# Kernel tuning notes

Hardware: AMD Instinct MI355X
Metric: run time of the kernel (lower is better)

Reference implementation:

```python
import jax, jax.numpy as jnp
import numpy as np

# Model constants (from init_kwargs)
B, S, D = 2, 2048, 2048          # batch, seq, d_model
E = 64                           # num_routed_experts
TOP_K = 4
BOT = int(D * 0.25)              # bottle_dim = 512
EXP = 1536                       # routed expert hidden (bigmac_expert_size)
DFF = 8192                       # shared expert hidden (d_ff)
Z_LOSS_W = 1e-4
MOE_SCALE = 0.5                  # 1/(1 + [num_shared_experts>0])


def setup_inputs() -> dict:
    key = jax.random.key(0)
    ks = jax.random.split(key, 10)
    std = 0.011
    return {
        "x": jax.random.normal(ks[0], (B, S, D), jnp.float32),
        "router_w": jax.random.normal(ks[1], (E, D), jnp.float32) * 0.02,
        "gate_w": jax.random.normal(ks[2], (DFF, D), jnp.float32) * std,
        "up_w": jax.random.normal(ks[3], (DFF, D), jnp.float32) * std,
        "down_w": jax.random.normal(ks[4], (D, DFF), jnp.float32) * std,
        "w_down": jax.random.normal(ks[5], (BOT, D), jnp.float32) * std,
        "w_up": jax.random.normal(ks[6], (D, BOT), jnp.float32) * std,
        "w12": jax.random.normal(ks[7], (E, BOT, 2 * EXP), jnp.float32) * std,
        "w3": jax.random.normal(ks[8], (E, EXP, BOT), jnp.float32) * std,
    }


def reference(x, router_w, gate_w, up_w, down_w, w_down, w_up, w12, w3):
    b, s, d = x.shape
    h = x.reshape(-1, d)                       # [N, D]
    N = h.shape[0]
    NT = N * TOP_K                             # total routed token-slots

    # ---- router (fp32) ----
    logits = h @ router_w.T                    # [N, E]
    scores = jax.nn.sigmoid(logits)
    z_loss = jnp.mean(jnp.nan_to_num(logits) ** 2) * Z_LOSS_W
    # expert_bias is None -> selection_scores == scores
    _, topk_idx = jax.lax.top_k(scores, TOP_K)             # [N, K]
    topk_logits = jnp.take_along_axis(logits, topk_idx, axis=1)
    gating = jax.nn.softmax(topk_logits, axis=-1)          # [N, K]

    # ---- shared expert (SwiGLU) ----
    shared = (jax.nn.silu(h @ gate_w.T) * (h @ up_w.T)) @ down_w.T  # [N, D]

    # ---- bottleneck down-projection ----
    down = h @ w_down.T                        # [N, BOT]

    # ---- dispatch: sort tokens by expert, capacity-limited padding ----
    flat = topk_idx.reshape(-1)                # [NT]
    order = jnp.argsort(flat)                  # stable sort
    sorted_e = flat[order]
    counts = jax.ops.segment_sum(jnp.ones(NT, jnp.int32), flat, num_segments=E)
    ptr = jnp.cumsum(counts) - counts          # expert start offsets
    local = jnp.arange(NT) - ptr[sorted_e]     # rank within expert
    max_load = (NT // E // 8 + 6) * 8          # capacity per expert
    num_slots = E * max_load
    mask = local < max_load
    slots = sorted_e * max_load + local
    token_idx = jnp.repeat(jnp.arange(N), TOP_K)

    # reverse_map[slot] = source token row (N = dummy row); extra slot absorbs dropped tokens
    rev = jnp.full(num_slots + 1, N, dtype=jnp.int32)
    rev = rev.at[jnp.where(mask, slots, num_slots)].set(token_idx[order].astype(jnp.int32))
    rev = rev[:num_slots]

    h_dummy = jnp.concatenate([down, jnp.zeros((1, BOT), down.dtype)], axis=0)
    padding = h_dummy[rev].reshape(E, max_load, BOT)

    # ---- grouped expert GEMMs ----
    h12 = jnp.einsum('eld,edf->elf', padding, w12)   # [E, max_load, 2*EXP]
    h1, h2 = jnp.split(h12, 2, axis=-1)
    po = jnp.einsum('elf,efd->eld', jax.nn.silu(h1) * h2, w3)  # [E, max_load, BOT]
    po = jnp.concatenate([po.reshape(-1, BOT), jnp.zeros((1, BOT), po.dtype)], axis=0)

    # ---- combine: gather back, weight by gating ----
    gm = jnp.full(NT, num_slots, dtype=jnp.int32)
    gm = gm.at[order].set(jnp.where(mask, slots, num_slots).astype(jnp.int32))
    gathered = po[gm].reshape(N, TOP_K, BOT)
    routed = jnp.einsum('nk,nkd->nd', gating, gathered) @ w_up.T  # [N, D]

    # eval mode: route_scale = 1.0, aux_loss = 0
    out = ((shared + routed) * MOE_SCALE).reshape(b, s, d)
    return out, z_loss
```

## Files before the change

### kernel.cpp

```cpp
#include <hip/hip_runtime.h>

#define DEV __device__ __forceinline__

typedef __attribute__((ext_vector_type(4))) float f4;
typedef __attribute__((ext_vector_type(8))) __bf16 bfrag;
typedef __attribute__((ext_vector_type(4))) unsigned short us4;
typedef __attribute__((ext_vector_type(8))) unsigned short us8;

#define NTOK   4096
#define DMODEL 2048
#define NEXP   64
#define MAXLD  304
#define NSLOT  19456

DEV unsigned short f2bf(float f){
  union { float f; unsigned int i; } u; u.f = f;
  unsigned int r = u.i + 0x7fffu + ((u.i >> 16) & 1u);
  return (unsigned short)(r >> 16);
}
DEV float bf2f(unsigned short b){
  union { unsigned int i; float f; } u; u.i = ((unsigned int)b) << 16;
  return u.f;
}

DEV void gl_lds16(const unsigned short* g, unsigned short* l){
  __builtin_amdgcn_global_load_lds(
      (const __attribute__((address_space(1))) void*)g,
      (__attribute__((address_space(3))) void*)l, 16, 0, 0);
}

template<int EPI>
__global__ __launch_bounds__(256) void gemm_bt(
    const unsigned short* __restrict__ A, const unsigned short* __restrict__ B,
    void* __restrict__ Cp, const float* __restrict__ addin,
    int M, int N, int K, long long sA, long long sB, long long sC)
{
  __shared__ unsigned short As[128*32];
  __shared__ unsigned short Bs[128*32];
  A += (long long)blockIdx.z * sA;
  B += (long long)blockIdx.z * sB;
  const long long cbase = (long long)blockIdx.z * sC;
  const int bm = blockIdx.y * 128, bn = blockIdx.x * 128;
  const int t = threadIdx.x, wave = t >> 6, lane = t & 63;
  const int wm = (wave >> 1) * 64, wn = (wave & 1) * 64;
  const int fr = lane & 15, kg = lane >> 4;

  f4 acc[4][4];
#pragma unroll
  for (int m = 0; m < 4; ++m)
#pragma unroll
    for (int n = 0; n < 4; ++n)
      acc[m][n] = f4{0.f, 0.f, 0.f, 0.f};

  const int i0 = t, i1 = 256 + t;
  int ar0 = bm + (i0 >> 2); if (ar0 > M - 1) ar0 = M - 1;
  int ar1 = bm + (i1 >> 2); if (ar1 > M - 1) ar1 = M - 1;
  int br0 = bn + (i0 >> 2); if (br0 > N - 1) br0 = N - 1;
  int br1 = bn + (i1 >> 2); if (br1 > N - 1) br1 = N - 1;
  const unsigned short* ap0 = A + (long long)ar0 * K + (i0 & 3) * 8;
  const unsigned short* ap1 = A + (long long)ar1 * K + (i1 & 3) * 8;
  const unsigned short* bp0 = B + (long long)br0 * K + (i0 & 3) * 8;
  const unsigned short* bp1 = B + (long long)br1 * K + (i1 & 3) * 8;
  unsigned short* da0 = As + wave * 512;
  unsigned short* da1 = As + 2048 + wave * 512;
  unsigned short* db0 = Bs + wave * 512;
  unsigned short* db1 = Bs + 2048 + wave * 512;

  for (int k0 = 0; k0 < K; k0 += 32){
    gl_lds16(ap0, da0);
    gl_lds16(ap1, da1);
    gl_lds16(bp0, db0);
    gl_lds16(bp1, db1);
    ap0 += 32; ap1 += 32; bp0 += 32; bp1 += 32;
    __syncthreads();
    bfrag af[4], bfv[4];
#pragma unroll
    for (int m = 0; m < 4; ++m) af[m] = *(const bfrag*)&As[(wm + m*16 + fr)*32 + kg*8];
#pragma unroll
    for (int n = 0; n < 4; ++n) bfv[n] = *(const bfrag*)&Bs[(wn + n*16 + fr)*32 + kg*8];
#pragma unroll
    for (int m = 0; m < 4; ++m)
#pragma unroll
      for (int n = 0; n < 4; ++n)
        acc[m][n] = __builtin_amdgcn_mfma_f32_16x16x32_bf16(af[m], bfv[n], acc[m][n], 0, 0, 0);
    __syncthreads();
  }

#pragma unroll
  for (int m = 0; m < 4; ++m){
    const int row0 = bm + wm + m*16 + kg*4;
#pragma unroll
    for (int n = 0; n < 4; ++n){
      const int col = bn + wn + n*16 + fr;
      if (col < N){
        f4 v = acc[m][n];
#pragma unroll
        for (int r = 0; r < 4; ++r){
          const int row = row0 + r;
          if (row < M){
            const long long off = cbase + (long long)row * N + col;
            if (EPI == 0)      ((unsigned short*)Cp)[off] = f2bf(v[r]);
            else if (EPI == 1) ((float*)Cp)[off] = v[r];
            else               ((float*)Cp)[off] = (v[r] + addin[off]) * 0.5f;
          }
        }
      }
    }
  }
}

__global__ void cvt_bf16(const float* __restrict__ in, unsigned short* __restrict__ out,
                         long long n4)
{
  long long i = (long long)blockIdx.x * 256 + threadIdx.x;
  if (i >= n4) return;
  float4 v = ((const float4*)in)[i];
  us4 o; o[0] = f2bf(v.x); o[1] = f2bf(v.y); o[2] = f2bf(v.z); o[3] = f2bf(v.w);
  ((us4*)out)[i] = o;
}

__global__ __launch_bounds__(256) void transpose_cvt(const float* __restrict__ in,
    unsigned short* __restrict__ out, int R, int C)
{
  __shared__ float tile[32][33];
  const long long z = blockIdx.z;
  const float* ip = in + z * (long long)R * C;
  unsigned short* op = out + z * (long long)R * C;
  const int r0 = blockIdx.y * 32, c0 = blockIdx.x * 32;
  const int t = threadIdx.x;
  const int lr = t >> 3, lc = (t & 7) * 4;
  float4 v = *(const float4*)(ip + (long long)(r0 + lr) * C + c0 + lc);
  tile[lr][lc+0] = v.x; tile[lr][lc+1] = v.y; tile[lr][lc+2] = v.z; tile[lr][lc+3] = v.w;
  __syncthreads();
  const int oc = t >> 3, orr = (t & 7) * 4;
  us4 o;
  o[0] = f2bf(tile[orr+0][oc]); o[1] = f2bf(tile[orr+1][oc]);
  o[2] = f2bf(tile[orr+2][oc]); o[3] = f2bf(tile[orr+3][oc]);
  *(us4*)(op + (long long)(c0 + oc) * R + r0 + orr) = o;
}

__global__ void router_topk(const float* __restrict__ logits, int* __restrict__ topk,
                            float* __restrict__ gating, float* __restrict__ zout)
{
  const int t = threadIdx.x, w = t >> 6, lane = t & 63;
  const int n = blockIdx.x * 4 + w;
  const float lg = logits[(long long)n * 64 + lane];
  float z = lg * lg;
#pragma unroll
  for (int off = 32; off; off >>= 1) z += __shfl_xor(z, off);
  __shared__ float zs[4];
  if (lane == 0) zs[w] = z;
  __syncthreads();
  if (t == 0) atomicAdd(zout, (zs[0]+zs[1]+zs[2]+zs[3]) * (0.0001f / 262144.0f));

  float cur = lg;
  float tl[4]; int ti[4];
#pragma unroll
  for (int k = 0; k < 4; ++k){
    float s = cur; int si = lane;
#pragma unroll
    for (int off = 32; off; off >>= 1){
      float so = __shfl_xor(s, off); int io = __shfl_xor(si, off);
      if (so > s || (so == s && io < si)){ s = so; si = io; }
    }
    tl[k] = s; ti[k] = si;
    if (lane == si) cur = -3.0e38f;
  }
  if (lane == 0){
    const float m0 = tl[0];
    const float e0 = __expf(tl[0]-m0), e1 = __expf(tl[1]-m0),
                e2 = __expf(tl[2]-m0), e3 = __expf(tl[3]-m0);
    const float inv = 1.0f / (e0 + e1 + e2 + e3);
    topk[n*4+0] = ti[0]; topk[n*4+1] = ti[1]; topk[n*4+2] = ti[2]; topk[n*4+3] = ti[3];
    gating[n*4+0] = e0*inv; gating[n*4+1] = e1*inv; gating[n*4+2] = e2*inv; gating[n*4+3] = e3*inv;
  }
}

__global__ void scan_route(const int* __restrict__ topk, int* __restrict__ gm,
                           int* __restrict__ rev, int* __restrict__ counts)
{
  const int e = blockIdx.x;
  const int t = threadIdx.x, w = t >> 6, lane = t & 63;
  __shared__ int wtot[4];
  int running = 0;
  for (int c = 0; c < 16384; c += 256){
    const int j = c + t;
    const bool p = (topk[j] == e);
    const unsigned long long m = __ballot(p);
    const int prefix = __popcll(m & ((1ull << lane) - 1ull));
    if (lane == 0) wtot[w] = __popcll(m);
    __syncthreads();
    int woff = 0;
#pragma unroll
    for (int i = 0; i < 4; ++i){ if (i < w) woff += wtot[i]; }
    const int btot = wtot[0] + wtot[1] + wtot[2] + wtot[3];
    if (p){
      const int rank = running + woff + prefix;
      gm[j] = (rank < MAXLD) ? (e * MAXLD + rank) : NSLOT;
      if (rank < MAXLD) rev[e * MAXLD + rank] = j >> 2;
    }
    running += btot;
    __syncthreads();
  }
  if (t == 0) counts[e] = running;
}

__global__ void gather_pad(const unsigned short* __restrict__ down, const int* __restrict__ rev,
                           const int* __restrict__ counts, unsigned short* __restrict__ pad)
{
  const int idx = blockIdx.x * 256 + threadIdx.x;
  const int s = idx >> 6, c8 = (idx & 63) * 8;
  const int e = s / MAXLD;
  const int r = s - e * MAXLD;
  int cnt = counts[e]; if (cnt > MAXLD) cnt = MAXLD;
  us8 v = {0,0,0,0,0,0,0,0};
  if (r < cnt){
    const int tok = rev[s];
    v = *(const us8*)(down + (long long)tok * 512 + c8);
  }
  *(us8*)(pad + (long long)s * 512 + c8) = v;
}

__global__ void silu_mul(const unsigned short* __restrict__ G, const unsigned short* __restrict__ U,
                         unsigned short* __restrict__ O, long long ldg, long long ldu, long long ldo,
                         long long cols8, long long total)
{
  const long long idx = (long long)blockIdx.x * 256 + threadIdx.x;
  if (idx >= total) return;
  const long long rr = idx / cols8;
  const long long cc = (idx - rr * cols8) * 8;
  us8 g = *(const us8*)(G + rr * ldg + cc);
  us8 u = *(const us8*)(U + rr * ldu + cc);
  us8 o;
#pragma unroll
  for (int j = 0; j < 8; ++j){
    const float gf = bf2f(g[j]);
    const float s = gf / (1.0f + __expf(-gf));
    o[j] = f2bf(s * bf2f(u[j]));
  }
  *(us8*)(O + rr * ldo + cc) = o;
}

__global__ void combine_moe(const unsigned short* __restrict__ po, const int* __restrict__ gm,
                            const float* __restrict__ gating, unsigned short* __restrict__ routed)
{
  const int idx = blockIdx.x * 256 + threadIdx.x;
  const int n = idx >> 6, c8 = (idx & 63) * 8;
  float acc[8] = {0,0,0,0,0,0,0,0};
#pragma unroll
  for (int k = 0; k < 4; ++k){
    const int slot = gm[n*4 + k];
    if (slot < NSLOT){
      const float gw = gating[n*4 + k];
      us8 v = *(const us8*)(po + (long long)slot * 512 + c8);
#pragma unroll
      for (int j = 0; j < 8; ++j) acc[j] += gw * bf2f(v[j]);
    }
  }
  us8 o;
#pragma unroll
  for (int j = 0; j < 8; ++j) o[j] = f2bf(acc[j]);
  *(us8*)(routed + (long long)n * 512 + c8) = o;
}

extern "C" void kernel_launch(void* const* d_in, const int* in_sizes, int n_in,
                              void* d_out, int out_size, void* d_ws, size_t ws_size,
                              hipStream_t stream)
{
  const float* x      = (const float*)d_in[0];
  const float* rw     = (const float*)d_in[1];
  const float* gate_w = (const float*)d_in[2];
  const float* up_w   = (const float*)d_in[3];
  const float* down_w = (const float*)d_in[4];
  const float* w_down = (const float*)d_in[5];
  const float* w_up   = (const float*)d_in[6];
  const float* w12    = (const float*)d_in[7];
  const float* w3     = (const float*)d_in[8];
  float* out = (float*)d_out;

  char* ws = (char*)d_ws;
  unsigned short* HBF   = (unsigned short*)(ws + 0ull);
  unsigned short* RWBF  = (unsigned short*)(ws + 16777216ull);
  unsigned short* GATEB = (unsigned short*)(ws + 17039360ull);
  unsigned short* UPB   = (unsigned short*)(ws + 50593792ull);
  unsigned short* DWB   = (unsigned short*)(ws + 84148224ull);
  unsigned short* WDB   = (unsigned short*)(ws + 117702656ull);
  unsigned short* WUB   = (unsigned short*)(ws + 119799808ull);
  unsigned short* W12T  = (unsigned short*)(ws + 121896960ull);
  unsigned short* W3T   = (unsigned short*)(ws + 323223552ull);
  float*          LOGIT = (float*)(ws + 423886848ull);
  int*            TOPKI = (int*)(ws + 424935424ull);
  float*          GATE4 = (float*)(ws + 425000960ull);
  int*            GM    = (int*)(ws + 425066496ull);
  int*            CNT   = (int*)(ws + 425132032ull);
  int*            REV   = (int*)(ws + 425132288ull);
  unsigned short* GU    = (unsigned short*)(ws + 425210112ull);
  unsigned short* ACTS  = (unsigned short*)(ws + 559427840ull);
  float*          SHRD  = (float*)(ws + 626536704ull);
  unsigned short* DNB   = (unsigned short*)(ws + 660091136ull);
  unsigned short* PAD   = (unsigned short*)(ws + 664285440ull);
  unsigned short* PO    = (unsigned short*)(ws + 684208384ull);
  unsigned short* RTD   = (unsigned short*)(ws + 704131328ull);

  hipMemsetAsync((char*)d_out + 8388608ull * 4, 0, 4, stream);

  cvt_bf16<<<8192,  256, 0, stream>>>(x,      HBF,   2097152);
  cvt_bf16<<<128,   256, 0, stream>>>(rw,     RWBF,  32768);
  cvt_bf16<<<16384, 256, 0, stream>>>(gate_w, GATEB, 4194304);
  cvt_bf16<<<16384, 256, 0, stream>>>(up_w,   UPB,   4194304);
  cvt_bf16<<<16384, 256, 0, stream>>>(down_w, DWB,   4194304);
  cvt_bf16<<<1024,  256, 0, stream>>>(w_down, WDB,   262144);
  cvt_bf16<<<1024,  256, 0, stream>>>(w_up,   WUB,   262144);
  transpose_cvt<<<dim3(96,16,64), 256, 0, stream>>>(w12, W12T, 512, 3072);
  transpose_cvt<<<dim3(16,48,64), 256, 0, stream>>>(w3,  W3T,  1536, 512);

  gemm_bt<1><<<dim3(1,32,1), 256, 0, stream>>>(HBF, RWBF, LOGIT, nullptr,
                                               4096, 64, 2048, 0, 0, 0);
  router_topk<<<1024, 256, 0, stream>>>(LOGIT, TOPKI, GATE4, out + 8388608);
  scan_route<<<64, 256, 0, stream>>>(TOPKI, GM, REV, CNT);

  gemm_bt<0><<<dim3(64,32,1), 256, 0, stream>>>(HBF, GATEB, GU, nullptr,
                                                4096, 8192, 2048, 0, 0, 0);
  gemm_bt<0><<<dim3(64,32,1), 256, 0, stream>>>(HBF, UPB, GU + 33554432ull, nullptr,
                                                4096, 8192, 2048, 0, 0, 0);
  silu_mul<<<16384, 256, 0, stream>>>(GU, GU + 33554432ull, ACTS, 8192, 8192, 8192,
                                      1024, 4194304);
  gemm_bt<1><<<dim3(16,32,1), 256, 0, stream>>>(ACTS, DWB, SHRD, nullptr,
                                                4096, 2048, 8192, 0, 0, 0);

  gemm_bt<0><<<dim3(4,32,1), 256, 0, stream>>>(HBF, WDB, DNB, nullptr,
                                               4096, 512, 2048, 0, 0, 0);
  gather_pad<<<4864, 256, 0, stream>>>(DNB, REV, CNT, PAD);
  gemm_bt<0><<<dim3(24,3,64), 256, 0, stream>>>(PAD, W12T, GU, nullptr,
                                                304, 3072, 512, 155648, 1572864, 933888);
  silu_mul<<<14592, 256, 0, stream>>>(GU, GU + 1536, ACTS, 3072, 3072, 1536,
                                      192, 3735552);
  gemm_bt<0><<<dim3(4,3,64), 256, 0, stream>>>(ACTS, W3T, PO, nullptr,
                                               304, 512, 1536, 466944, 786432, 155648);
  combine_moe<<<1024, 256, 0, stream>>>(PO, GM, GATE4, RTD);

  gemm_bt<2><<<dim3(16,32,1), 256, 0, stream>>>(RTD, WUB, out, SHRD,
                                                4096, 2048, 512, 0, 0, 0);
}
```

Baseline: 1.346 ms.

## Add 256x256-tile triple-buffered GEMM kernel for shared-expert projections

Introduces a new 512-thread GEMM with 256x256 output tiles, a three-stage LDS ring fed by global_load_lds, XOR-swizzled LDS layout, grid remapping for L2 locality, and MFMA priority hints. It replaces the 128x128 GEMM for the three large shared-expert SwiGLU matmuls. The larger tiles raise arithmetic intensity and the deeper pipeline overlaps loads with MFMA. In exchange it uses heavy register and LDS pressure (96KB LDS per block), and the down-projection grid shrinks to 128 blocks, which may underfill the CUs.

Result: faster. 1.261 ms (-6.3%).

```diff
diff --git a/kernel.cpp b/kernel.cpp
--- a/kernel.cpp
+++ b/kernel.cpp
@@ -27,6 +27,130 @@
   __builtin_amdgcn_global_load_lds(
       (const __attribute__((address_space(1))) void*)g,
       (__attribute__((address_space(3))) void*)l, 16, 0, 0);
+}
+
+template<int EPI>
+__global__ __launch_bounds__(512, 2) void gemm256(
+    const unsigned short* __restrict__ A, const unsigned short* __restrict__ B,
+    void* __restrict__ Cp, int M, int N, int K)
+{
+  __shared__ unsigned short As[3][256*32];
+  __shared__ unsigned short Bs[3][256*32];
+
+  const int nwg = gridDim.x * gridDim.y;
+  int bid = blockIdx.y * gridDim.x + blockIdx.x;
+  bid = (bid & 7) * (nwg >> 3) + (bid >> 3);
+  const int bx = bid % gridDim.x, by = bid / gridDim.x;
+  const int bm = by * 256, bn = bx * 256;
+
+  const int t = threadIdx.x, lane = t & 63;
+  const int wave = t >> 6;
+  const int wm = (wave >> 2) * 128, wn = (wave & 3) * 64;
+  const int fr = lane & 15, kg = lane >> 4;
+
+  const int p0 = t, p1 = t + 512;
+  const int ar0 = p0 >> 2, as0 = (p0 & 3) ^ ((ar0 >> 1) & 3);
+  const int ar1 = p1 >> 2, as1 = (p1 & 3) ^ ((ar1 >> 1) & 3);
+  const unsigned short* a0 = A + (long long)(bm + ar0) * K + as0 * 8;
+  const unsigned short* a1 = A + (long long)(bm + ar1) * K + as1 * 8;
+  const unsigned short* b0 = B + (long long)(bn + ar0) * K + as0 * 8;
+  const unsigned short* b1 = B + (long long)(bn + ar1) * K + as1 * 8;
+
+  f4 acc[8][4];
+#pragma unroll
+  for (int m = 0; m < 8; ++m)
+#pragma unroll
+    for (int n = 0; n < 4; ++n) acc[m][n] = f4{0.f,0.f,0.f,0.f};
+
+  const int nt = K >> 5;
+
+  gl_lds16(a0, &As[0][p0*8]); gl_lds16(a1, &As[0][p1*8]);
+  gl_lds16(b0, &Bs[0][p0*8]); gl_lds16(b1, &Bs[0][p1*8]);
+  a0 += 32; a1 += 32; b0 += 32; b1 += 32;
+  gl_lds16(a0, &As[1][p0*8]); gl_lds16(a1, &As[1][p1*8]);
+  gl_lds16(b0, &Bs[1][p0*8]); gl_lds16(b1, &Bs[1][p1*8]);
+  a0 += 32; a1 += 32; b0 += 32; b1 += 32;
+  asm volatile("s_waitcnt vmcnt(4)" ::: "memory");
+  __builtin_amdgcn_s_barrier();
+  __builtin_amdgcn_sched_barrier(0);
+
+  int cur = 0;
+  for (int tt = 0; tt < nt; ++tt){
+    const unsigned short* Ab = As[cur];
+    const unsigned short* Bb = Bs[cur];
+    const int stg = (cur >= 1) ? cur - 1 : cur + 2;
+    const bool do_stage = (tt + 2 < nt);
+
+    bfrag bf[4];
+#pragma unroll
+    for (int n = 0; n < 4; ++n){
+      const int r = wn + n*16 + fr;
+      bf[n] = *(const bfrag*)&Bb[r*32 + ((kg ^ ((r>>1)&3)) << 3)];
+    }
+
+    bfrag af[4];
+#pragma unroll
+    for (int m = 0; m < 4; ++m){
+      const int r = wm + m*16 + fr;
+      af[m] = *(const bfrag*)&Ab[r*32 + ((kg ^ ((r>>1)&3)) << 3)];
+    }
+    if (do_stage){
+      gl_lds16(a0, &As[stg][p0*8]); gl_lds16(a1, &As[stg][p1*8]);
+      a0 += 32; a1 += 32;
+    }
+    __builtin_amdgcn_s_setprio(1);
+#pragma unroll
+    for (int m = 0; m < 4; ++m)
+#pragma unroll
+      for (int n = 0; n < 4; ++n)
+        acc[m][n] = __builtin_amdgcn_mfma_f32_16x16x32_bf16(af[m], bf[n], acc[m][n], 0, 0, 0);
+    __builtin_amdgcn_s_setprio(0);
+
+#pragma unroll
+    for (int m = 0; m < 4; ++m){
+      const int r = wm + 64 + m*16 + fr;
+      af[m] = *(const bfrag*)&Ab[r*32 + ((kg ^ ((r>>1)&3)) << 3)];
+    }
+    if (do_stage){
+      gl_lds16(b0, &Bs[stg][p0*8]); gl_lds16(b1, &Bs[stg][p1*8]);
+      b0 += 32; b1 += 32;
+    }
+    __builtin_amdgcn_s_setprio(1);
+#pragma unroll
+    for (int m = 0; m < 4; ++m)
+#pragma unroll
+      for (int n = 0; n < 4; ++n)
+        acc[4+m][n] = __builtin_amdgcn_mfma_f32_16x16x32_bf16(af[m], bf[n], acc[4+m][n], 0, 0, 0);
+    __builtin_amdgcn_s_setprio(0);
+
+    __builtin_amdgcn_sched_barrier(0);
+    if (tt + 2 < nt){
+      asm volatile("s_waitcnt vmcnt(4)" ::: "memory");
+    } else if (tt + 1 < nt){
+      asm volatile("s_waitcnt vmcnt(0)" ::: "memory");
+    }
+    if (tt + 1 < nt){
+      __builtin_amdgcn_s_barrier();
+      __builtin_amdgcn_sched_barrier(0);
+    }
+    cur = (cur == 2) ? 0 : cur + 1;
+  }
+
+#pragma unroll
+  for (int m = 0; m < 8; ++m){
+    const int row0 = bm + wm + m*16 + kg*4;
+#pragma unroll
+    for (int n = 0; n < 4; ++n){
+      const int col = bn + wn + n*16 + fr;
+      f4 v = acc[m][n];
+#pragma unroll
+      for (int r = 0; r < 4; ++r){
+        const long long off = (long long)(row0 + r) * N + col;
+        if (EPI == 0) ((unsigned short*)Cp)[off] = f2bf(v[r]);
+        else          ((float*)Cp)[off] = v[r];
+      }
+    }
+  }
 }
 
 template<int EPI>
@@ -319,14 +443,11 @@
   router_topk<<<1024, 256, 0, stream>>>(LOGIT, TOPKI, GATE4, out + 8388608);
   scan_route<<<64, 256, 0, stream>>>(TOPKI, GM, REV, CNT);
 
-  gemm_bt<0><<<dim3(64,32,1), 256, 0, stream>>>(HBF, GATEB, GU, nullptr,
-                                                4096, 8192, 2048, 0, 0, 0);
-  gemm_bt<0><<<dim3(64,32,1), 256, 0, stream>>>(HBF, UPB, GU + 33554432ull, nullptr,
-                                                4096, 8192, 2048, 0, 0, 0);
+  gemm256<0><<<dim3(32,16), 512, 0, stream>>>(HBF, GATEB, GU, 4096, 8192, 2048);
+  gemm256<0><<<dim3(32,16), 512, 0, stream>>>(HBF, UPB, GU + 33554432ull, 4096, 8192, 2048);
   silu_mul<<<16384, 256, 0, stream>>>(GU, GU + 33554432ull, ACTS, 8192, 8192, 8192,
                                       1024, 4194304);
-  gemm_bt<1><<<dim3(16,32,1), 256, 0, stream>>>(ACTS, DWB, SHRD, nullptr,
-                                                4096, 2048, 8192, 0, 0, 0);
+  gemm256<1><<<dim3(8,16), 512, 0, stream>>>(ACTS, DWB, SHRD, 4096, 2048, 8192);
 
   gemm_bt<0><<<dim3(4,32,1), 256, 0, stream>>>(HBF, WDB, DNB, nullptr,
                                                4096, 512, 2048, 0, 0, 0);
```

## Add 8-wave 256-wide pipelined GEMM kernel for shared-expert and output projections

Applied to the files above, without the earlier changes.

Adds a new 512-thread GEMM kernel with 256x256 or 128x256 tiles, double-buffered LDS with direct global-to-LDS loads, XOR-swizzled LDS layout, interleaved MFMA/load phases with priority hints, and XCD-aware block remapping. It replaces the 128x128 kernel for the shared expert gate/up/down GEMMs and the final up projection. The goal is more data reuse per tile and overlap of memory traffic with MFMA work on the dominant dense GEMMs. In exchange it uses more LDS and registers per block, and it relies on M and N being exact multiples of the larger tiles.

After: 1.211 ms. 10.0% less time.

```diff
diff --git a/kernel.cpp b/kernel.cpp
--- a/kernel.cpp
+++ b/kernel.cpp
@@ -27,6 +27,176 @@
   __builtin_amdgcn_global_load_lds(
       (const __attribute__((address_space(1))) void*)g,
       (__attribute__((address_space(3))) void*)l, 16, 0, 0);
+}
+
+template<int BM, int EPI>
+__global__ __launch_bounds__(512, 2) void gemm8p(
+    const unsigned short* __restrict__ A, const unsigned short* __restrict__ B,
+    void* __restrict__ Cp, const float* __restrict__ addin, int M, int N, int K)
+{
+  constexpr int FM  = BM / 32;
+  constexpr int HV  = FM / 2;
+  constexpr int ALD = BM / 128;
+  __shared__ unsigned short As[2][2][BM * 32];
+  __shared__ unsigned short Bs[2][2][256 * 32];
+
+  const int nwg = gridDim.x * gridDim.y;
+  int bid = blockIdx.y * gridDim.x + blockIdx.x;
+  bid = (bid & 7) * (nwg >> 3) + (bid >> 3);
+  const int bx = bid % gridDim.x, by = bid / gridDim.x;
+  const int bm = by * BM, bn = bx * 256;
+
+  const int t = threadIdx.x, lane = t & 63, wave = t >> 6;
+  const int wm = (wave >> 2) * (BM / 2), wn = (wave & 3) * 64;
+  const int fr = lane & 15, kg = lane >> 4;
+
+  const int sw = ((t >> 3) & 3) ^ (t & 3);
+  const unsigned short* a_src0 = A + (long long)(bm + (t >> 2)) * K + sw * 8;
+  const unsigned short* a_src1 = A + (long long)(bm + (t >> 2) + 128) * K + sw * 8;
+  const unsigned short* b_src0 = B + (long long)(bn + (t >> 2)) * K + sw * 8;
+  const unsigned short* b_src1 = B + (long long)(bn + (t >> 2) + 128) * K + sw * 8;
+  const int wch = wave * 64;
+
+#define STG_A(bufv, ksv, koff) do { \
+    gl_lds16(a_src0 + (koff) + (ksv) * 32, &As[bufv][ksv][wch * 8]); \
+    if (ALD == 2) gl_lds16(a_src1 + (koff) + (ksv) * 32, &As[bufv][ksv][(512 + wch) * 8]); \
+  } while (0)
+#define STG_B(bufv, ksv, koff) do { \
+    gl_lds16(b_src0 + (koff) + (ksv) * 32, &Bs[bufv][ksv][wch * 8]); \
+    gl_lds16(b_src1 + (koff) + (ksv) * 32, &Bs[bufv][ksv][(512 + wch) * 8]); \
+  } while (0)
+#define WAIT_LPT() do { if (ALD == 2) asm volatile("s_waitcnt vmcnt(4)" ::: "memory"); \
+                        else          asm volatile("s_waitcnt vmcnt(3)" ::: "memory"); } while (0)
+#define WAIT_ZERO() asm volatile("s_waitcnt vmcnt(0)" ::: "memory")
+#define LGKM0() do { asm volatile("s_waitcnt lgkmcnt(0)" ::: "memory"); \
+                     __builtin_amdgcn_sched_barrier(0); } while (0)
+
+  f4 acc[FM][4];
+#pragma unroll
+  for (int m = 0; m < FM; ++m)
+#pragma unroll
+    for (int n = 0; n < 4; ++n) acc[m][n] = f4{0.f, 0.f, 0.f, 0.f};
+
+  const int nt = K >> 6;
+
+  STG_A(0, 0, 0); STG_B(0, 0, 0); STG_A(0, 1, 0); STG_B(0, 1, 0);
+  WAIT_LPT();
+  __builtin_amdgcn_s_barrier();
+  __builtin_amdgcn_sched_barrier(0);
+
+  int buf = 0;
+  for (int tt = 0; tt < nt; ++tt){
+    const long long ko = (long long)(tt + 1) * 64;
+    const bool stg = (tt + 1 < nt);
+    const int nb = buf ^ 1;
+    bfrag bfv[4], af[HV];
+
+#pragma unroll
+    for (int n = 0; n < 4; ++n){
+      const int r = wn + n * 16 + fr;
+      bfv[n] = *(const bfrag*)&Bs[buf][0][r * 32 + ((kg ^ ((r >> 1) & 3)) << 3)];
+    }
+#pragma unroll
+    for (int m = 0; m < HV; ++m){
+      const int r = wm + m * 16 + fr;
+      af[m] = *(const bfrag*)&As[buf][0][r * 32 + ((kg ^ ((r >> 1) & 3)) << 3)];
+    }
+    if (stg) STG_A(nb, 0, ko);
+    __builtin_amdgcn_s_barrier();
+    LGKM0();
+    __builtin_amdgcn_s_setprio(1);
+#pragma unroll
+    for (int m = 0; m < HV; ++m)
+#pragma unroll
+      for (int n = 0; n < 4; ++n)
+        acc[m][n] = __builtin_amdgcn_mfma_f32_16x16x32_bf16(af[m], bfv[n], acc[m][n], 0, 0, 0);
+    __builtin_amdgcn_s_setprio(0);
+    __builtin_amdgcn_s_barrier();
+
+#pragma unroll
+    for (int m = 0; m < HV; ++m){
+      const int r = wm + HV * 16 + m * 16 + fr;
+      af[m] = *(const bfrag*)&As[buf][0][r * 32 + ((kg ^ ((r >> 1) & 3)) << 3)];
+    }
+    if (stg) STG_B(nb, 0, ko);
+    __builtin_amdgcn_s_barrier();
+    LGKM0();
+    __builtin_amdgcn_s_setprio(1);
+#pragma unroll
+    for (int m = 0; m < HV; ++m)
+#pragma unroll
+      for (int n = 0; n < 4; ++n)
+        acc[HV + m][n] = __builtin_amdgcn_mfma_f32_16x16x32_bf16(af[m], bfv[n], acc[HV + m][n], 0, 0, 0);
+    __builtin_amdgcn_s_setprio(0);
+    if (stg) WAIT_LPT(); else WAIT_ZERO();
+    __builtin_amdgcn_s_barrier();
+    __builtin_amdgcn_sched_barrier(0);
+
+#pragma unroll
+    for (int n = 0; n < 4; ++n){
+      const int r = wn + n * 16 + fr;
+      bfv[n] = *(const bfrag*)&Bs[buf][1][r * 32 + ((kg ^ ((r >> 1) & 3)) << 3)];
+    }
+#pragma unroll
+    for (int m = 0; m < HV; ++m){
+      const int r = wm + m * 16 + fr;
+      af[m] = *(const bfrag*)&As[buf][1][r * 32 + ((kg ^ ((r >> 1) & 3)) << 3)];
+    }
+    if (stg) STG_A(nb, 1, ko);
+    __builtin_amdgcn_s_barrier();
+    LGKM0();
+    __builtin_amdgcn_s_setprio(1);
+#pragma unroll
+    for (int m = 0; m < HV; ++m)
+#pragma unroll
+      for (int n = 0; n < 4; ++n)
+        acc[m][n] = __builtin_amdgcn_mfma_f32_16x16x32_bf16(af[m], bfv[n], acc[m][n], 0, 0, 0);
+    __builtin_amdgcn_s_setprio(0);
+    __builtin_amdgcn_s_barrier();
+
+#pragma unroll
+    for (int m = 0; m < HV; ++m){
+      const int r = wm + HV * 16 + m * 16 + fr;
+      af[m] = *(const bfrag*)&As[buf][1][r * 32 + ((kg ^ ((r >> 1) & 3)) << 3)];
+    }
+    if (stg) STG_B(nb, 1, ko);
+    __builtin_amdgcn_s_barrier();
+    LGKM0();
+    __builtin_amdgcn_s_setprio(1);
+#pragma unroll
+    for (int m = 0; m < HV; ++m)
+#pragma unroll
+      for (int n = 0; n < 4; ++n)
+        acc[HV + m][n] = __builtin_amdgcn_mfma_f32_16x16x32_bf16(af[m], bfv[n], acc[HV + m][n], 0, 0, 0);
+    __builtin_amdgcn_s_setprio(0);
+    if (stg) WAIT_LPT();
+    __builtin_amdgcn_s_barrier();
+    __builtin_amdgcn_sched_barrier(0);
+
+    buf = nb;
+  }
+
+#pragma unroll
+  for (int m = 0; m < FM; ++m){
+    const int row0 = bm + wm + m * 16 + kg * 4;
+#pragma unroll
+    for (int n = 0; n < 4; ++n){
+      const int col = bn + wn + n * 16 + fr;
+      f4 v = acc[m][n];
+#pragma unroll
+      for (int r = 0; r < 4; ++r){
+        const long long off = (long long)(row0 + r) * N + col;
+        if (EPI == 0)      ((unsigned short*)Cp)[off] = f2bf(v[r]);
+        else if (EPI == 1) ((float*)Cp)[off] = v[r];
+        else               ((float*)Cp)[off] = (v[r] + addin[off]) * 0.5f;
+      }
+    }
+  }
+#undef STG_A
+#undef STG_B
+#undef WAIT_LPT
+#undef WAIT_ZERO
+#undef LGKM0
 }
 
 template<int EPI>
@@ -319,14 +489,11 @@
   router_topk<<<1024, 256, 0, stream>>>(LOGIT, TOPKI, GATE4, out + 8388608);
   scan_route<<<64, 256, 0, stream>>>(TOPKI, GM, REV, CNT);
 
-  gemm_bt<0><<<dim3(64,32,1), 256, 0, stream>>>(HBF, GATEB, GU, nullptr,
-                                                4096, 8192, 2048, 0, 0, 0);
-  gemm_bt<0><<<dim3(64,32,1), 256, 0, stream>>>(HBF, UPB, GU + 33554432ull, nullptr,
-                                                4096, 8192, 2048, 0, 0, 0);
+  gemm8p<256,0><<<dim3(32,16), 512, 0, stream>>>(HBF, GATEB, GU, nullptr, 4096, 8192, 2048);
+  gemm8p<256,0><<<dim3(32,16), 512, 0, stream>>>(HBF, UPB, GU + 33554432ull, nullptr, 4096, 8192, 2048);
   silu_mul<<<16384, 256, 0, stream>>>(GU, GU + 33554432ull, ACTS, 8192, 8192, 8192,
                                       1024, 4194304);
-  gemm_bt<1><<<dim3(16,32,1), 256, 0, stream>>>(ACTS, DWB, SHRD, nullptr,
-                                                4096, 2048, 8192, 0, 0, 0);
+  gemm8p<128,1><<<dim3(8,32), 512, 0, stream>>>(ACTS, DWB, SHRD, nullptr, 4096, 2048, 8192);
 
   gemm_bt<0><<<dim3(4,32,1), 256, 0, stream>>>(HBF, WDB, DNB, nullptr,
                                                4096, 512, 2048, 0, 0, 0);
@@ -339,6 +506,5 @@
                                                304, 512, 1536, 466944, 786432, 155648);
   combine_moe<<<1024, 256, 0, stream>>>(PO, GM, GATE4, RTD);
 
-  gemm_bt<2><<<dim3(16,32,1), 256, 0, stream>>>(RTD, WUB, out, SHRD,
-                                                4096, 2048, 512, 0, 0, 0);
-}
+  gemm8p<128,2><<<dim3(8,32), 512, 0, stream>>>(RTD, WUB, out, SHRD, 4096, 2048, 512);
+}
```

## Add 4-stage pipelined large-tile GEMM for shared expert and output projections

Applied to the files above, without the earlier changes.

Introduces a new 512-thread GEMM kernel with 256-wide N tiles and a 4-buffer LDS ring. It issues global-to-LDS loads three stages ahead, uses an XOR swizzle against bank conflicts, remaps workgroups for locality, and raises wave priority around the MFMA blocks. The dense shared-expert gate/up/down GEMMs and the final output projection now use it in place of the older 128x128 kernel, to hide memory latency and improve data reuse. The cost is much more LDS per block and hand-tuned vmcnt waits that depend on exact load counts, which could limit occupancy or break if shapes change.

After: 1.152 ms. 14.4% less time.

```diff
diff --git a/kernel.cpp b/kernel.cpp
--- a/kernel.cpp
+++ b/kernel.cpp
@@ -27,6 +27,114 @@
   __builtin_amdgcn_global_load_lds(
       (const __attribute__((address_space(1))) void*)g,
       (__attribute__((address_space(3))) void*)l, 16, 0, 0);
+}
+
+template<int BM, int EPI>
+__global__ __launch_bounds__(512, 2) void gemmdp(
+    const unsigned short* __restrict__ A, const unsigned short* __restrict__ B,
+    void* __restrict__ Cp, const float* __restrict__ addin, int M, int N, int K)
+{
+  constexpr int FM  = BM / 32;
+  constexpr int ALD = BM / 128;
+  __shared__ unsigned short As[4][BM * 32];
+  __shared__ unsigned short Bs[4][256 * 32];
+
+  const int nwg = gridDim.x * gridDim.y;
+  int bid = blockIdx.y * gridDim.x + blockIdx.x;
+  bid = (bid & 7) * (nwg >> 3) + (bid >> 3);
+  const int bx = bid % gridDim.x, by = bid / gridDim.x;
+  const int bm = by * BM, bn = bx * 256;
+
+  const int t = threadIdx.x, lane = t & 63, wave = t >> 6;
+  const int wm = (wave >> 2) * (BM / 2), wn = (wave & 3) * 64;
+  const int fr = lane & 15, kg = lane >> 4;
+
+  const int sw = ((t >> 3) & 3) ^ (t & 3);
+  const unsigned short* a_src0 = A + (long long)(bm + (t >> 2)) * K + sw * 8;
+  const unsigned short* a_src1 = A + (long long)(bm + (t >> 2) + 128) * K + sw * 8;
+  const unsigned short* b_src0 = B + (long long)(bn + (t >> 2)) * K + sw * 8;
+  const unsigned short* b_src1 = B + (long long)(bn + (t >> 2) + 128) * K + sw * 8;
+  const int wch = wave * 64;
+
+#define STG(bv, tt_) do { const long long ko_ = (long long)(tt_) * 32;            \
+    gl_lds16(a_src0 + ko_, &As[bv][wch * 8]);                                     \
+    if (ALD == 2) gl_lds16(a_src1 + ko_, &As[bv][(512 + wch) * 8]);               \
+    gl_lds16(b_src0 + ko_, &Bs[bv][wch * 8]);                                     \
+    gl_lds16(b_src1 + ko_, &Bs[bv][(512 + wch) * 8]); } while (0)
+
+  f4 acc[FM][4];
+#pragma unroll
+  for (int m = 0; m < FM; ++m)
+#pragma unroll
+    for (int n = 0; n < 4; ++n) acc[m][n] = f4{0.f, 0.f, 0.f, 0.f};
+
+  const int nt = K >> 5;
+
+  STG(0, 0); STG(1, 1); STG(2, 2);
+  if constexpr (ALD == 2) asm volatile("s_waitcnt vmcnt(8)" ::: "memory");
+  else                    asm volatile("s_waitcnt vmcnt(6)" ::: "memory");
+  __builtin_amdgcn_s_barrier();
+  __builtin_amdgcn_sched_barrier(0);
+
+  for (int tt = 0; tt < nt; ++tt){
+    const unsigned short* Ab = As[tt & 3];
+    const unsigned short* Bb = Bs[tt & 3];
+    bfrag bfv[4], af[FM];
+#pragma unroll
+    for (int n = 0; n < 4; ++n){
+      const int r = wn + n * 16 + fr;
+      bfv[n] = *(const bfrag*)&Bb[r * 32 + ((kg ^ ((r >> 1) & 3)) << 3)];
+    }
+#pragma unroll
+    for (int m = 0; m < FM; ++m){
+      const int r = wm + m * 16 + fr;
+      af[m] = *(const bfrag*)&Ab[r * 32 + ((kg ^ ((r >> 1) & 3)) << 3)];
+    }
+    if (tt + 3 < nt) STG((tt + 3) & 3, tt + 3);
+    asm volatile("s_waitcnt lgkmcnt(0)" ::: "memory");
+    __builtin_amdgcn_sched_barrier(0);
+    __builtin_amdgcn_s_setprio(1);
+#pragma unroll
+    for (int m = 0; m < FM; ++m)
+#pragma unroll
+      for (int n = 0; n < 4; ++n)
+        acc[m][n] = __builtin_amdgcn_mfma_f32_16x16x32_bf16(af[m], bfv[n], acc[m][n], 0, 0, 0);
+    __builtin_amdgcn_s_setprio(0);
+    __builtin_amdgcn_sched_barrier(0);
+
+    const int rem = nt - 2 - tt;
+    if constexpr (ALD == 2){
+      if (rem >= 2)      asm volatile("s_waitcnt vmcnt(8)" ::: "memory");
+      else if (rem == 1) asm volatile("s_waitcnt vmcnt(4)" ::: "memory");
+      else if (rem == 0) asm volatile("s_waitcnt vmcnt(0)" ::: "memory");
+    } else {
+      if (rem >= 2)      asm volatile("s_waitcnt vmcnt(6)" ::: "memory");
+      else if (rem == 1) asm volatile("s_waitcnt vmcnt(3)" ::: "memory");
+      else if (rem == 0) asm volatile("s_waitcnt vmcnt(0)" ::: "memory");
+    }
+    if (tt + 1 < nt){
+      __builtin_amdgcn_s_barrier();
+      __builtin_amdgcn_sched_barrier(0);
+    }
+  }
+
+#pragma unroll
+  for (int m = 0; m < FM; ++m){
+    const int row0 = bm + wm + m * 16 + kg * 4;
+#pragma unroll
+    for (int n = 0; n < 4; ++n){
+      const int col = bn + wn + n * 16 + fr;
+      f4 v = acc[m][n];
+#pragma unroll
+      for (int r = 0; r < 4; ++r){
+        const long long off = (long long)(row0 + r) * N + col;
+        if (EPI == 0)      ((unsigned short*)Cp)[off] = f2bf(v[r]);
+        else if (EPI == 1) ((float*)Cp)[off] = v[r];
+        else               ((float*)Cp)[off] = (v[r] + addin[off]) * 0.5f;
+      }
+    }
+  }
+#undef STG
 }
 
 template<int EPI>
@@ -319,14 +427,11 @@
   router_topk<<<1024, 256, 0, stream>>>(LOGIT, TOPKI, GATE4, out + 8388608);
   scan_route<<<64, 256, 0, stream>>>(TOPKI, GM, REV, CNT);
 
-  gemm_bt<0><<<dim3(64,32,1), 256, 0, stream>>>(HBF, GATEB, GU, nullptr,
-                                                4096, 8192, 2048, 0, 0, 0);
-  gemm_bt<0><<<dim3(64,32,1), 256, 0, stream>>>(HBF, UPB, GU + 33554432ull, nullptr,
-                                                4096, 8192, 2048, 0, 0, 0);
+  gemmdp<256,0><<<dim3(32,16), 512, 0, stream>>>(HBF, GATEB, GU, nullptr, 4096, 8192, 2048);
+  gemmdp<256,0><<<dim3(32,16), 512, 0, stream>>>(HBF, UPB, GU + 33554432ull, nullptr, 4096, 8192, 2048);
   silu_mul<<<16384, 256, 0, stream>>>(GU, GU + 33554432ull, ACTS, 8192, 8192, 8192,
                                       1024, 4194304);
-  gemm_bt<1><<<dim3(16,32,1), 256, 0, stream>>>(ACTS, DWB, SHRD, nullptr,
-                                                4096, 2048, 8192, 0, 0, 0);
+  gemmdp<128,1><<<dim3(8,32), 512, 0, stream>>>(ACTS, DWB, SHRD, nullptr, 4096, 2048, 8192);
 
   gemm_bt<0><<<dim3(4,32,1), 256, 0, stream>>>(HBF, WDB, DNB, nullptr,
                                                4096, 512, 2048, 0, 0, 0);
@@ -339,6 +444,5 @@
                                                304, 512, 1536, 466944, 786432, 155648);
   combine_moe<<<1024, 256, 0, stream>>>(PO, GM, GATE4, RTD);
 
-  gemm_bt<2><<<dim3(16,32,1), 256, 0, stream>>>(RTD, WUB, out, SHRD,
-                                                4096, 2048, 512, 0, 0, 0);
-}
+  gemmdp<128,2><<<dim3(8,32), 512, 0, stream>>>(RTD, WUB, out, SHRD, 4096, 2048, 512);
+}
```
